# Kernel tuning notes

Measured on AMD Instinct MI355X. Metric: run time of the kernel, lower is better.

## Reference

```python
import jax, jax.numpy as jnp
import numpy as np

EMBED_DIM = 1024
NUM_HEADS = 16
HEAD_DIM = EMBED_DIM // NUM_HEADS
SCALE = HEAD_DIM ** -0.5


def setup_inputs() -> dict:
    key = jax.random.key(0)
    ks = jax.random.split(key, 8)
    B, N = 4, 2048
    x = jax.random.normal(ks[0], (B, N, EMBED_DIM), dtype=jnp.float32)
    rope_cos = jax.random.uniform(ks[1], (N, HEAD_DIM), dtype=jnp.float32)
    rope_sin = jax.random.uniform(ks[2], (N, HEAD_DIM), dtype=jnp.float32)
    # Learned params (torch nn.Linear: y = x @ W.T + b); store W as [in, out]
    s_qkv = 1.0 / np.sqrt(EMBED_DIM)
    W_qkv = jax.random.uniform(ks[3], (EMBED_DIM, 3 * EMBED_DIM), dtype=jnp.float32, minval=-s_qkv, maxval=s_qkv)
    b_qkv = jax.random.uniform(ks[4], (3 * EMBED_DIM,), dtype=jnp.float32, minval=-s_qkv, maxval=s_qkv)
    W_proj = jax.random.uniform(ks[5], (EMBED_DIM, EMBED_DIM), dtype=jnp.float32, minval=-s_qkv, maxval=s_qkv)
    b_proj = jax.random.uniform(ks[6], (EMBED_DIM,), dtype=jnp.float32, minval=-s_qkv, maxval=s_qkv)
    return {"x": x, "rope_cos": rope_cos, "rope_sin": rope_sin,
            "W_qkv": W_qkv, "b_qkv": b_qkv, "W_proj": W_proj, "b_proj": b_proj}


def _rotate_half(t):
    t1, t2 = jnp.split(t, 2, axis=-1)
    return jnp.concatenate((-t2, t1), axis=-1)


def reference(x, rope_cos, rope_sin, W_qkv, b_qkv, W_proj, b_proj):
    B, N, D = x.shape
    qkv = x @ W_qkv + b_qkv                       # [B, N, 3D]
    qkv = qkv.reshape(B, N, 3, NUM_HEADS, HEAD_DIM)
    qkv = jnp.transpose(qkv, (2, 0, 3, 1, 4))     # [3, B, H, N, hd]
    q, k, v = qkv[0], qkv[1], qkv[2]
    cos = rope_cos[None, None]                    # [1, 1, N, hd]
    sin = rope_sin[None, None]
    q = q * cos + _rotate_half(q) * sin
    k = k * cos + _rotate_half(k) * sin
    attn = jnp.einsum('bhqd,bhkd->bhqk', q, k) * SCALE
    attn = jax.nn.softmax(attn, axis=-1)
    out = jnp.einsum('bhqk,bhkd->bhqd', attn, v)  # [B, H, N, hd]
    out = jnp.transpose(out, (0, 2, 1, 3)).reshape(B, N, D)
    return out @ W_proj + b_proj
```

## Files before the change

kernel.cpp:

```cpp
#include <hip/hip_runtime.h>
#include <stdint.h>

#define EMBED 1024
#define NHEAD 16
#define HD    64
#define SEQ   2048
#define BATCH 4

typedef __bf16 bf16x8 __attribute__((ext_vector_type(8)));
typedef __bf16 bf16x2t __attribute__((ext_vector_type(2)));
typedef float  f32x4  __attribute__((ext_vector_type(4)));
typedef unsigned int u32x2 __attribute__((ext_vector_type(2)));
typedef unsigned int u32x4 __attribute__((ext_vector_type(4)));

#define GLB(p)  ((__attribute__((address_space(1))) unsigned int*)(p))
#define LDSP(p) ((__attribute__((address_space(3))) unsigned int*)(p))
#define MFMA(a,b,c) __builtin_amdgcn_mfma_f32_16x16x32_bf16(a,b,c,0,0,0)
#define EXP2(x) __builtin_amdgcn_exp2f(x)

#define QSCALE 0.18033688011112042f

__device__ __forceinline__ unsigned int f2bf(float f) {
    unsigned int u = __float_as_uint(f);
    return (u + 0x7FFFu + ((u >> 16) & 1u)) >> 16;
}
__device__ __forceinline__ unsigned int pack2(float a, float b) {
    return f2bf(a) | (f2bf(b) << 16);
}
__device__ __forceinline__ unsigned int cvtpk(float lo, float hi) {
    bf16x2t w; w[0] = (__bf16)lo; w[1] = (__bf16)hi;
    return __builtin_bit_cast(unsigned int, w);
}

__device__ __forceinline__ void pswap32(unsigned int &a, unsigned int &b) {
#if __has_builtin(__builtin_amdgcn_permlane32_swap)
    u32x2 r = __builtin_amdgcn_permlane32_swap(a, b, false, false);
    a = r[0]; b = r[1];
#else
    unsigned int sa = (unsigned int)__shfl_xor((int)a, 32);
    unsigned int sb = (unsigned int)__shfl_xor((int)b, 32);
    bool hi = (threadIdx.x & 32) != 0;
    unsigned int na = hi ? sb : a;
    unsigned int nb = hi ? b : sa;
    a = na; b = nb;
#endif
}
__device__ __forceinline__ void pswap16(unsigned int &a, unsigned int &b) {
#if __has_builtin(__builtin_amdgcn_permlane16_swap)
    u32x2 r = __builtin_amdgcn_permlane16_swap(a, b, false, false);
    a = r[0]; b = r[1];
#else
    unsigned int sa = (unsigned int)__shfl_xor((int)a, 16);
    unsigned int sb = (unsigned int)__shfl_xor((int)b, 16);
    bool oddq = (threadIdx.x & 16) != 0;
    unsigned int na = oddq ? sb : a;
    unsigned int nb = oddq ? b : sa;
    a = na; b = nb;
#endif
}
__device__ __forceinline__ void pswap_q(unsigned int &a, unsigned int &b) {
    pswap32(a, b);
    pswap16(a, b);
}

__global__ void k_convert(const float* __restrict__ in, unsigned short* __restrict__ out, int n4) {
    int i = blockIdx.x * 256 + threadIdx.x;
    if (i >= n4) return;
    f32x4 v = ((const f32x4*)in)[i];
    u32x2 w = { pack2(v[0], v[1]), pack2(v[2], v[3]) };
    ((u32x2*)out)[i] = w;
}

__global__ void k_transpose(const float* __restrict__ in, unsigned short* __restrict__ out, int K, int C) {
    __shared__ float t[32][33];
    int c0 = blockIdx.x * 32, k0 = blockIdx.y * 32;
    int tid = threadIdx.x;
    #pragma unroll
    for (int i = 0; i < 4; i++) {
        int e = tid + i * 256;
        t[e >> 5][e & 31] = in[(size_t)(k0 + (e >> 5)) * C + c0 + (e & 31)];
    }
    __syncthreads();
    #pragma unroll
    for (int i = 0; i < 4; i++) {
        int e = tid + i * 256;
        int cl = e >> 5, kl = e & 31;
        out[(size_t)(c0 + cl) * K + k0 + kl] = (unsigned short)f2bf(t[kl][cl]);
    }
}

__global__ __launch_bounds__(256) void k_qkv(const unsigned short* __restrict__ xb,
    const unsigned short* __restrict__ wt, const float* __restrict__ bias,
    const float* __restrict__ rc, const float* __restrict__ rs,
    unsigned short* __restrict__ Qb, unsigned short* __restrict__ Kb, unsigned short* __restrict__ Vt)
{
    __shared__ unsigned short Al[128 * 32];
    __shared__ unsigned short Bl[128 * 32];
    const int tid = threadIdx.x;
    const int wave = tid >> 6, lane = tid & 63;
    const int l15 = lane & 15, l4 = lane >> 4;
    const int wr = wave >> 1, wc = wave & 1;
    const int tm = blockIdx.y * 128, tc = blockIdx.x * 128;

    const int srow = wave * 32 + (lane >> 2);
    const int scol = (lane & 3) * 8;
    const unsigned short* ga = xb + (size_t)(tm + srow) * EMBED + scol;
    const unsigned short* gb = wt + (size_t)(tc + srow) * EMBED + scol;

    f32x4 acc[4][4] = {};
    for (int k0 = 0; k0 < EMBED; k0 += 32) {
        __syncthreads();
        __builtin_amdgcn_global_load_lds(GLB(ga + k0),               LDSP(Al + wave * 1024),       16, 0, 0);
        __builtin_amdgcn_global_load_lds(GLB(ga + k0 + 16 * EMBED),  LDSP(Al + wave * 1024 + 512), 16, 0, 0);
        __builtin_amdgcn_global_load_lds(GLB(gb + k0),               LDSP(Bl + wave * 1024),       16, 0, 0);
        __builtin_amdgcn_global_load_lds(GLB(gb + k0 + 16 * EMBED),  LDSP(Bl + wave * 1024 + 512), 16, 0, 0);
        __syncthreads();
        bf16x8 af[4], bfr[4];
        #pragma unroll
        for (int m = 0; m < 4; m++) af[m]  = *(const bf16x8*)&Al[(wr * 64 + m * 16 + l15) * 32 + l4 * 8];
        #pragma unroll
        for (int n = 0; n < 4; n++) bfr[n] = *(const bf16x8*)&Bl[(wc * 64 + n * 16 + l15) * 32 + l4 * 8];
        #pragma unroll
        for (int m = 0; m < 4; m++)
            #pragma unroll
            for (int n = 0; n < 4; n++)
                acc[m][n] = MFMA(af[m], bfr[n], acc[m][n]);
    }

    const int cb = tc + wc * 64;
    const int s = cb >> 10;
    const int h = (cb >> 6) & 15;
    if (s < 2) {
        #pragma unroll
        for (int m = 0; m < 4; m++)
            #pragma unroll
            for (int j = 0; j < 4; j++) {
                int row = tm + wr * 64 + m * 16 + l4 * 4 + j;
                int b = row >> 11, pos = row & (SEQ - 1);
                float v[4];
                #pragma unroll
                for (int n = 0; n < 4; n++) v[n] = acc[m][n][j] + bias[cb + n * 16 + l15];
                float o[4];
                #pragma unroll
                for (int p = 0; p < 2; p++) {
                    int d1 = p * 16 + l15;
                    float c1 = rc[pos * HD + d1],      s1 = rs[pos * HD + d1];
                    float c2 = rc[pos * HD + d1 + 32], s2 = rs[pos * HD + d1 + 32];
                    o[p]     = v[p] * c1     - v[p + 2] * s1;
                    o[p + 2] = v[p + 2] * c2 + v[p] * s2;
                }
                float mul = (s == 0) ? QSCALE : 1.0f;
                unsigned short* dst = (s == 0 ? Qb : Kb) + ((size_t)(b * NHEAD + h) * SEQ + pos) * HD;
                #pragma unroll
                for (int n = 0; n < 4; n++) dst[n * 16 + l15] = (unsigned short)f2bf(o[n] * mul);
            }
    } else {
        #pragma unroll
        for (int m = 0; m < 4; m++) {
            int row0 = tm + wr * 64 + m * 16 + l4 * 4;
            int b = row0 >> 11, pos0 = row0 & (SEQ - 1);
            #pragma unroll
            for (int n = 0; n < 4; n++) {
                float bb = bias[cb + n * 16 + l15];
                u32x2 w = { pack2(acc[m][n][0] + bb, acc[m][n][1] + bb),
                            pack2(acc[m][n][2] + bb, acc[m][n][3] + bb) };
                *(u32x2*)(Vt + ((size_t)(b * NHEAD + h) * HD + n * 16 + l15) * SEQ + pos0) = w;
            }
        }
    }
}

__global__ __launch_bounds__(256) void k_attn(const unsigned short* __restrict__ Qb,
    const unsigned short* __restrict__ Kb, const unsigned short* __restrict__ Vt,
    unsigned short* __restrict__ O)
{
    __shared__ unsigned short Kl[2][64 * 64];
    __shared__ unsigned short Vl[2][64 * 64];
    const int tid = threadIdx.x, wave = tid >> 6, lane = tid & 63;
    const int l15 = lane & 15, l4 = lane >> 4;
    const int bh = blockIdx.y;
    const int b = bh >> 4, h = bh & 15;
    const int q0 = blockIdx.x * 128 + wave * 32;

    const unsigned short* Qg = Qb + ((size_t)bh * SEQ + q0) * HD;
    bf16x8 qf[2][2];
    #pragma unroll
    for (int qb = 0; qb < 2; qb++)
        #pragma unroll
        for (int ds = 0; ds < 2; ds++)
            qf[qb][ds] = *(const bf16x8*)(Qg + (qb * 16 + l15) * HD + ds * 32 + l4 * 8);

    const int srow = lane >> 3;
    const int selem = ((lane & 7) * 8) ^ ((srow & 7) * 8);
    const unsigned short* kg = Kb + (size_t)bh * SEQ * HD + (size_t)(wave * 16 + srow) * HD + selem;
    const unsigned short* vg = Vt + (size_t)bh * HD * SEQ + (size_t)(wave * 16 + srow) * SEQ + selem;

#define ISSUE(kt_, bi_) do { \
    __builtin_amdgcn_global_load_lds(GLB(kg + (size_t)(kt_) * HD),       LDSP(&Kl[bi_][0] + wave * 1024),       16, 0, 0); \
    __builtin_amdgcn_global_load_lds(GLB(kg + (size_t)((kt_) + 8) * HD), LDSP(&Kl[bi_][0] + wave * 1024 + 512), 16, 0, 0); \
    __builtin_amdgcn_global_load_lds(GLB(vg + (kt_)),                    LDSP(&Vl[bi_][0] + wave * 1024),       16, 0, 0); \
    __builtin_amdgcn_global_load_lds(GLB(vg + 8 * SEQ + (kt_)),          LDSP(&Vl[bi_][0] + wave * 1024 + 512), 16, 0, 0); \
} while (0)

    f32x4 accO[2][4] = {};
    float mst[2] = { -1e30f, -1e30f }, lst[2] = { 0.f, 0.f };

    ISSUE(0, 0);

    for (int kt = 0; kt < SEQ; kt += 64) {
        const int cur = (kt >> 6) & 1;
        asm volatile("s_waitcnt vmcnt(0)" ::: "memory");
        __builtin_amdgcn_s_barrier();
        if (kt + 64 < SEQ) ISSUE(kt + 64, cur ^ 1);
        __builtin_amdgcn_sched_barrier(0);

        const unsigned short* Klc = &Kl[cur][0];
        const unsigned short* Vlc = &Vl[cur][0];

        f32x4 sacc[2][4] = {};
        __builtin_amdgcn_s_setprio(1);
        #pragma unroll
        for (int ds = 0; ds < 2; ds++)
            #pragma unroll
            for (int kb = 0; kb < 4; kb++) {
                int krow = kb * 16 + l15;
                bf16x8 kf = *(const bf16x8*)((const char*)Klc + krow * 128 + ((ds * 64 + l4 * 16) ^ ((krow & 7) << 4)));
                sacc[0][kb] = MFMA(kf, qf[0][ds], sacc[0][kb]);
                sacc[1][kb] = MFMA(kf, qf[1][ds], sacc[1][kb]);
            }
        __builtin_amdgcn_s_setprio(0);

        bf16x8 pf[2][2];
        #pragma unroll
        for (int qb = 0; qb < 2; qb++) {
            float pm = -1e30f;
            #pragma unroll
            for (int kb = 0; kb < 4; kb++)
                #pragma unroll
                for (int r = 0; r < 4; r++) pm = fmaxf(pm, sacc[qb][kb][r]);
            pm = fmaxf(pm, __shfl_xor(pm, 16));
            pm = fmaxf(pm, __shfl_xor(pm, 32));
            bool skip = __all(pm <= mst[qb] + 8.f);
            float mnew = skip ? mst[qb] : fmaxf(mst[qb], pm);
            float ls = 0.f;
            unsigned int w[4][2];
            #pragma unroll
            for (int kb = 0; kb < 4; kb++) {
                float p0 = EXP2(sacc[qb][kb][0] - mnew);
                float p1 = EXP2(sacc[qb][kb][1] - mnew);
                float p2 = EXP2(sacc[qb][kb][2] - mnew);
                float p3 = EXP2(sacc[qb][kb][3] - mnew);
                ls += (p0 + p1) + (p2 + p3);
                w[kb][0] = cvtpk(p0, p1);
                w[kb][1] = cvtpk(p2, p3);
            }
            ls += __shfl_xor(ls, 16);
            ls += __shfl_xor(ls, 32);
            if (skip) {
                lst[qb] += ls;
            } else {
                float corr = EXP2(mst[qb] - mnew);
                mst[qb] = mnew;
                lst[qb] = lst[qb] * corr + ls;
                #pragma unroll
                for (int db = 0; db < 4; db++) accO[qb][db] *= corr;
            }
            pswap_q(w[0][0], w[1][0]);
            pswap_q(w[0][1], w[1][1]);
            pswap_q(w[2][0], w[3][0]);
            pswap_q(w[2][1], w[3][1]);
            u32x4 f0 = { w[0][0], w[0][1], w[1][0], w[1][1] };
            u32x4 f1 = { w[2][0], w[2][1], w[3][0], w[3][1] };
            pf[qb][0] = __builtin_bit_cast(bf16x8, f0);
            pf[qb][1] = __builtin_bit_cast(bf16x8, f1);
        }

        __builtin_amdgcn_s_setprio(1);
        #pragma unroll
        for (int ds = 0; ds < 2; ds++)
            #pragma unroll
            for (int db = 0; db < 4; db++) {
                int vrow = db * 16 + l15;
                bf16x8 vf = *(const bf16x8*)((const char*)Vlc + vrow * 128 + ((ds * 64 + l4 * 16) ^ ((vrow & 7) << 4)));
                accO[0][db] = MFMA(vf, pf[0][ds], accO[0][db]);
                accO[1][db] = MFMA(vf, pf[1][ds], accO[1][db]);
            }
        __builtin_amdgcn_s_setprio(0);
    }
#undef ISSUE

    #pragma unroll
    for (int qb = 0; qb < 2; qb++) {
        float inv = 1.f / lst[qb];
        int tok = q0 + qb * 16 + l15;
        size_t rowo = ((size_t)b * SEQ + tok) * EMBED + h * HD;
        #pragma unroll
        for (int db = 0; db < 4; db++) {
            u32x2 w = { pack2(accO[qb][db][0] * inv, accO[qb][db][1] * inv),
                        pack2(accO[qb][db][2] * inv, accO[qb][db][3] * inv) };
            *(u32x2*)(O + rowo + db * 16 + l4 * 4) = w;
        }
    }
}

__global__ __launch_bounds__(256) void k_proj(const unsigned short* __restrict__ A,
    const unsigned short* __restrict__ wt, const float* __restrict__ bias, float* __restrict__ out)
{
    __shared__ unsigned short Al[128 * 32];
    __shared__ unsigned short Bl[128 * 32];
    const int tid = threadIdx.x;
    const int wave = tid >> 6, lane = tid & 63;
    const int l15 = lane & 15, l4 = lane >> 4;
    const int wr = wave >> 1, wc = wave & 1;
    const int tm = blockIdx.y * 128, tc = blockIdx.x * 128;

    const int srow = wave * 32 + (lane >> 2);
    const int scol = (lane & 3) * 8;
    const unsigned short* ga = A  + (size_t)(tm + srow) * EMBED + scol;
    const unsigned short* gb = wt + (size_t)(tc + srow) * EMBED + scol;

    f32x4 acc[4][4] = {};
    for (int k0 = 0; k0 < EMBED; k0 += 32) {
        __syncthreads();
        __builtin_amdgcn_global_load_lds(GLB(ga + k0),              LDSP(Al + wave * 1024),       16, 0, 0);
        __builtin_amdgcn_global_load_lds(GLB(ga + k0 + 16 * EMBED), LDSP(Al + wave * 1024 + 512), 16, 0, 0);
        __builtin_amdgcn_global_load_lds(GLB(gb + k0),              LDSP(Bl + wave * 1024),       16, 0, 0);
        __builtin_amdgcn_global_load_lds(GLB(gb + k0 + 16 * EMBED), LDSP(Bl + wave * 1024 + 512), 16, 0, 0);
        __syncthreads();
        bf16x8 af[4], bfr[4];
        #pragma unroll
        for (int m = 0; m < 4; m++) af[m]  = *(const bf16x8*)&Al[(wr * 64 + m * 16 + l15) * 32 + l4 * 8];
        #pragma unroll
        for (int n = 0; n < 4; n++) bfr[n] = *(const bf16x8*)&Bl[(wc * 64 + n * 16 + l15) * 32 + l4 * 8];
        #pragma unroll
        for (int m = 0; m < 4; m++)
            #pragma unroll
            for (int n = 0; n < 4; n++)
                acc[m][n] = MFMA(af[m], bfr[n], acc[m][n]);
    }

    #pragma unroll
    for (int m = 0; m < 4; m++)
        #pragma unroll
        for (int j = 0; j < 4; j++) {
            int row = tm + wr * 64 + m * 16 + l4 * 4 + j;
            #pragma unroll
            for (int n = 0; n < 4; n++) {
                int col = tc + wc * 64 + n * 16 + l15;
                out[(size_t)row * EMBED + col] = acc[m][n][j] + bias[col];
            }
        }
}

extern "C" void kernel_launch(void* const* d_in, const int* in_sizes, int n_in,
                              void* d_out, int out_size, void* d_ws, size_t ws_size,
                              hipStream_t stream) {
    const float* x     = (const float*)d_in[0];
    const float* rc    = (const float*)d_in[1];
    const float* rs    = (const float*)d_in[2];
    const float* Wqkv  = (const float*)d_in[3];
    const float* bqkv  = (const float*)d_in[4];
    const float* Wproj = (const float*)d_in[5];
    const float* bproj = (const float*)d_in[6];
    char* ws = (char*)d_ws;
    unsigned short* xb  = (unsigned short*)(ws);
    unsigned short* wqt = (unsigned short*)(ws + 16777216);
    unsigned short* wpt = (unsigned short*)(ws + 23068672);
    unsigned short* Qb  = (unsigned short*)(ws + 25165824);
    unsigned short* Kb  = (unsigned short*)(ws + 41943040);
    unsigned short* Vt  = (unsigned short*)(ws + 58720256);
    float* outp = (float*)d_out;

    k_convert  <<<8192, 256, 0, stream>>>(x, xb, 2097152);
    k_transpose<<<dim3(96, 32), 256, 0, stream>>>(Wqkv, wqt, 1024, 3072);
    k_transpose<<<dim3(32, 32), 256, 0, stream>>>(Wproj, wpt, 1024, 1024);
    k_qkv      <<<dim3(24, 64), 256, 0, stream>>>(xb, wqt, bqkv, rc, rs, Qb, Kb, Vt);
    k_attn     <<<dim3(16, 64), 256, 0, stream>>>(Qb, Kb, Vt, xb);
    k_proj     <<<dim3(8, 64),  256, 0, stream>>>(xb, wpt, bproj, outp);
}
```

Before: 339.6 us.

## Double-buffer GEMM LDS tiles and use permlane reductions in softmax

The QKV and projection GEMMs now keep two LDS buffers and issue the next k-tile's global-to-LDS loads right after a single barrier, so the fetch overlaps the MFMAs on the current tile. This replaces the old pattern of two syncthreads per iteration with no prefetch. In the attention softmax, the row max and sum reductions use three-input fmax trees and permlane32/16 swaps instead of shfl_xor, aiming to cut instruction latency. The cost is twice the LDS per block, which may lower occupancy, and the full vmcnt(0) wait still drains the loads each iteration.

Measured after the change: 329.9 us. 2.8% less time.

```diff
diff --git a/kernel.cpp b/kernel.cpp
--- a/kernel.cpp
+++ b/kernel.cpp
@@ -17,6 +17,7 @@
 #define LDSP(p) ((__attribute__((address_space(3))) unsigned int*)(p))
 #define MFMA(a,b,c) __builtin_amdgcn_mfma_f32_16x16x32_bf16(a,b,c,0,0,0)
 #define EXP2(x) __builtin_amdgcn_exp2f(x)
+#define F3(a,b,c) fmaxf(fmaxf((a),(b)),(c))
 
 #define QSCALE 0.18033688011112042f
 
@@ -62,6 +63,22 @@
     pswap32(a, b);
     pswap16(a, b);
 }
+__device__ __forceinline__ float red_max4(float x) {
+    unsigned int a = __float_as_uint(x), b = a;
+    pswap32(a, b);
+    float y = fmaxf(__uint_as_float(a), __uint_as_float(b));
+    unsigned int c = __float_as_uint(y), d = c;
+    pswap16(c, d);
+    return fmaxf(__uint_as_float(c), __uint_as_float(d));
+}
+__device__ __forceinline__ float red_sum4(float x) {
+    unsigned int a = __float_as_uint(x), b = a;
+    pswap32(a, b);
+    float y = __uint_as_float(a) + __uint_as_float(b);
+    unsigned int c = __float_as_uint(y), d = c;
+    pswap16(c, d);
+    return __uint_as_float(c) + __uint_as_float(d);
+}
 
 __global__ void k_convert(const float* __restrict__ in, unsigned short* __restrict__ out, int n4) {
     int i = blockIdx.x * 256 + threadIdx.x;
@@ -94,8 +111,8 @@
     const float* __restrict__ rc, const float* __restrict__ rs,
     unsigned short* __restrict__ Qb, unsigned short* __restrict__ Kb, unsigned short* __restrict__ Vt)
 {
-    __shared__ unsigned short Al[128 * 32];
-    __shared__ unsigned short Bl[128 * 32];
+    __shared__ unsigned short Al[2][128 * 32];
+    __shared__ unsigned short Bl[2][128 * 32];
     const int tid = threadIdx.x;
     const int wave = tid >> 6, lane = tid & 63;
     const int l15 = lane & 15, l4 = lane >> 4;
@@ -107,25 +124,35 @@
     const unsigned short* ga = xb + (size_t)(tm + srow) * EMBED + scol;
     const unsigned short* gb = wt + (size_t)(tc + srow) * EMBED + scol;
 
+#define GISSUE(k0_, bi_) do { \
+    __builtin_amdgcn_global_load_lds(GLB(ga + (k0_)),              LDSP(&Al[bi_][0] + wave * 1024),       16, 0, 0); \
+    __builtin_amdgcn_global_load_lds(GLB(ga + (k0_) + 16 * EMBED), LDSP(&Al[bi_][0] + wave * 1024 + 512), 16, 0, 0); \
+    __builtin_amdgcn_global_load_lds(GLB(gb + (k0_)),              LDSP(&Bl[bi_][0] + wave * 1024),       16, 0, 0); \
+    __builtin_amdgcn_global_load_lds(GLB(gb + (k0_) + 16 * EMBED), LDSP(&Bl[bi_][0] + wave * 1024 + 512), 16, 0, 0); \
+} while (0)
+
     f32x4 acc[4][4] = {};
+    GISSUE(0, 0);
     for (int k0 = 0; k0 < EMBED; k0 += 32) {
-        __syncthreads();
-        __builtin_amdgcn_global_load_lds(GLB(ga + k0),               LDSP(Al + wave * 1024),       16, 0, 0);
-        __builtin_amdgcn_global_load_lds(GLB(ga + k0 + 16 * EMBED),  LDSP(Al + wave * 1024 + 512), 16, 0, 0);
-        __builtin_amdgcn_global_load_lds(GLB(gb + k0),               LDSP(Bl + wave * 1024),       16, 0, 0);
-        __builtin_amdgcn_global_load_lds(GLB(gb + k0 + 16 * EMBED),  LDSP(Bl + wave * 1024 + 512), 16, 0, 0);
-        __syncthreads();
+        const int cur = (k0 >> 5) & 1;
+        asm volatile("s_waitcnt vmcnt(0)" ::: "memory");
+        __builtin_amdgcn_s_barrier();
+        if (k0 + 32 < EMBED) GISSUE(k0 + 32, cur ^ 1);
+        __builtin_amdgcn_sched_barrier(0);
+        const unsigned short* Ac = &Al[cur][0];
+        const unsigned short* Bc = &Bl[cur][0];
         bf16x8 af[4], bfr[4];
         #pragma unroll
-        for (int m = 0; m < 4; m++) af[m]  = *(const bf16x8*)&Al[(wr * 64 + m * 16 + l15) * 32 + l4 * 8];
-        #pragma unroll
-        for (int n = 0; n < 4; n++) bfr[n] = *(const bf16x8*)&Bl[(wc * 64 + n * 16 + l15) * 32 + l4 * 8];
+        for (int m = 0; m < 4; m++) af[m]  = *(const bf16x8*)&Ac[(wr * 64 + m * 16 + l15) * 32 + l4 * 8];
+        #pragma unroll
+        for (int n = 0; n < 4; n++) bfr[n] = *(const bf16x8*)&Bc[(wc * 64 + n * 16 + l15) * 32 + l4 * 8];
         #pragma unroll
         for (int m = 0; m < 4; m++)
             #pragma unroll
             for (int n = 0; n < 4; n++)
                 acc[m][n] = MFMA(af[m], bfr[n], acc[m][n]);
     }
+#undef GISSUE
 
     const int cb = tc + wc * 64;
     const int s = cb >> 10;
@@ -233,16 +260,20 @@
         bf16x8 pf[2][2];
         #pragma unroll
         for (int qb = 0; qb < 2; qb++) {
-            float pm = -1e30f;
-            #pragma unroll
-            for (int kb = 0; kb < 4; kb++)
-                #pragma unroll
-                for (int r = 0; r < 4; r++) pm = fmaxf(pm, sacc[qb][kb][r]);
-            pm = fmaxf(pm, __shfl_xor(pm, 16));
-            pm = fmaxf(pm, __shfl_xor(pm, 32));
+            float pm;
+            {
+                f32x4 s0 = sacc[qb][0], s1 = sacc[qb][1], s2 = sacc[qb][2], s3 = sacc[qb][3];
+                float t0 = F3(s0[0], s0[1], s0[2]);
+                float t1 = F3(s0[3], s1[0], s1[1]);
+                float t2 = F3(s1[2], s1[3], s2[0]);
+                float t3 = F3(s2[1], s2[2], s2[3]);
+                float t4 = F3(s3[0], s3[1], s3[2]);
+                pm = fmaxf(F3(t0, t1, t2), F3(t3, t4, s3[3]));
+            }
+            pm = red_max4(pm);
             bool skip = __all(pm <= mst[qb] + 8.f);
             float mnew = skip ? mst[qb] : fmaxf(mst[qb], pm);
-            float ls = 0.f;
+            float sk[4];
             unsigned int w[4][2];
             #pragma unroll
             for (int kb = 0; kb < 4; kb++) {
@@ -250,12 +281,12 @@
                 float p1 = EXP2(sacc[qb][kb][1] - mnew);
                 float p2 = EXP2(sacc[qb][kb][2] - mnew);
                 float p3 = EXP2(sacc[qb][kb][3] - mnew);
-                ls += (p0 + p1) + (p2 + p3);
+                sk[kb] = (p0 + p1) + (p2 + p3);
                 w[kb][0] = cvtpk(p0, p1);
                 w[kb][1] = cvtpk(p2, p3);
             }
-            ls += __shfl_xor(ls, 16);
-            ls += __shfl_xor(ls, 32);
+            float ls = (sk[0] + sk[1]) + (sk[2] + sk[3]);
+            ls = red_sum4(ls);
             if (skip) {
                 lst[qb] += ls;
             } else {
@@ -306,8 +337,8 @@
 __global__ __launch_bounds__(256) void k_proj(const unsigned short* __restrict__ A,
     const unsigned short* __restrict__ wt, const float* __restrict__ bias, float* __restrict__ out)
 {
-    __shared__ unsigned short Al[128 * 32];
-    __shared__ unsigned short Bl[128 * 32];
+    __shared__ unsigned short Al[2][128 * 32];
+    __shared__ unsigned short Bl[2][128 * 32];
     const int tid = threadIdx.x;
     const int wave = tid >> 6, lane = tid & 63;
     const int l15 = lane & 15, l4 = lane >> 4;
@@ -319,25 +350,35 @@
     const unsigned short* ga = A  + (size_t)(tm + srow) * EMBED + scol;
     const unsigned short* gb = wt + (size_t)(tc + srow) * EMBED + scol;
 
+#define GISSUE(k0_, bi_) do { \
+    __builtin_amdgcn_global_load_lds(GLB(ga + (k0_)),              LDSP(&Al[bi_][0] + wave * 1024),       16, 0, 0); \
+    __builtin_amdgcn_global_load_lds(GLB(ga + (k0_) + 16 * EMBED), LDSP(&Al[bi_][0] + wave * 1024 + 512), 16, 0, 0); \
+    __builtin_amdgcn_global_load_lds(GLB(gb + (k0_)),              LDSP(&Bl[bi_][0] + wave * 1024),       16, 0, 0); \
+    __builtin_amdgcn_global_load_lds(GLB(gb + (k0_) + 16 * EMBED), LDSP(&Bl[bi_][0] + wave * 1024 + 512), 16, 0, 0); \
+} while (0)
+
     f32x4 acc[4][4] = {};
+    GISSUE(0, 0);
     for (int k0 = 0; k0 < EMBED; k0 += 32) {
-        __syncthreads();
-        __builtin_amdgcn_global_load_lds(GLB(ga + k0),              LDSP(Al + wave * 1024),       16, 0, 0);
-        __builtin_amdgcn_global_load_lds(GLB(ga + k0 + 16 * EMBED), LDSP(Al + wave * 1024 + 512), 16, 0, 0);
-        __builtin_amdgcn_global_load_lds(GLB(gb + k0),              LDSP(Bl + wave * 1024),       16, 0, 0);
-        __builtin_amdgcn_global_load_lds(GLB(gb + k0 + 16 * EMBED), LDSP(Bl + wave * 1024 + 512), 16, 0, 0);
-        __syncthreads();
+        const int cur = (k0 >> 5) & 1;
+        asm volatile("s_waitcnt vmcnt(0)" ::: "memory");
+        __builtin_amdgcn_s_barrier();
+        if (k0 + 32 < EMBED) GISSUE(k0 + 32, cur ^ 1);
+        __builtin_amdgcn_sched_barrier(0);
+        const unsigned short* Ac = &Al[cur][0];
+        const unsigned short* Bc = &Bl[cur][0];
         bf16x8 af[4], bfr[4];
         #pragma unroll
-        for (int m = 0; m < 4; m++) af[m]  = *(const bf16x8*)&Al[(wr * 64 + m * 16 + l15) * 32 + l4 * 8];
-        #pragma unroll
-        for (int n = 0; n < 4; n++) bfr[n] = *(const bf16x8*)&Bl[(wc * 64 + n * 16 + l15) * 32 + l4 * 8];
+        for (int m = 0; m < 4; m++) af[m]  = *(const bf16x8*)&Ac[(wr * 64 + m * 16 + l15) * 32 + l4 * 8];
+        #pragma unroll
+        for (int n = 0; n < 4; n++) bfr[n] = *(const bf16x8*)&Bc[(wc * 64 + n * 16 + l15) * 32 + l4 * 8];
         #pragma unroll
         for (int m = 0; m < 4; m++)
             #pragma unroll
             for (int n = 0; n < 4; n++)
                 acc[m][n] = MFMA(af[m], bfr[n], acc[m][n]);
     }
+#undef GISSUE
 
     #pragma unroll
     for (int m = 0; m < 4; m++)
```
